# Performance work log

Measured on AMD Instinct MI355X. Metric: run time of the kernel, lower is better.

Reference implementation:

```python
import jax, jax.numpy as jnp
import numpy as np

D = 2048  # input_dim == hidden_dim (mult=1)
B = 16
C = 8.0   # self.c


def setup_inputs() -> dict:
    key = jax.random.key(0)
    k = jax.random.split(key, 5)
    # kaiming_normal fan_in, sigmoid gain = 1 -> std = 1/sqrt(fan_in)
    Wa = jax.random.normal(k[0], (D, D), dtype=jnp.float32) / np.sqrt(D)
    Wx = jax.random.normal(k[1], (D, D), dtype=jnp.float32) / np.sqrt(D)
    ba = jnp.zeros((D,), dtype=jnp.float32)
    bx = jnp.zeros((D,), dtype=jnp.float32)
    lo, hi = float(np.log(0.9 / 0.1)), float(np.log(0.999 / 0.001))  # logit(0.9), logit(0.999)
    Lam = jax.random.uniform(k[2], (D,), dtype=jnp.float32, minval=lo, maxval=hi)
    xt = jax.random.normal(k[3], (B, D), dtype=jnp.float32)
    ht_minus_1 = jax.random.normal(k[4], (B, D), dtype=jnp.float32)
    return {"xt": xt, "ht_minus_1": ht_minus_1, "Wa": Wa, "Wx": Wx,
            "ba": ba, "bx": bx, "Lam": Lam}


def reference(xt, ht_minus_1, Wa, Wx, ba, bx, Lam):
    # gates
    rt = jax.nn.sigmoid(xt @ Wa.T + ba)            # [B, H]
    it = jax.nn.sigmoid(xt @ Wx.T + bx)            # [B, H]
    log_a = -jax.nn.softplus(-Lam)                 # [H]
    a = jnp.exp(log_a * rt / C)                    # [B, H]
    # diag_embed(a): [B, H, H] with a on the diagonal (faithful to torch code)
    at = a[:, :, None] * jnp.eye(D, dtype=a.dtype)
    u = jnp.sqrt(1.0 - a * a) * (it * xt)          # [B, H]
    # torch broadcasting: [B,H,H] * [B,H] -> ht_minus_1/u broadcast over rows
    ht = at * ht_minus_1[:, None, :] + u[:, None, :]  # [B, H, H]
    return ht
```

## Files before the change

### kernel.cpp

```cpp
#include <hip/hip_runtime.h>

#define DD 2048
#define BB 16

typedef float f32x4 __attribute__((ext_vector_type(4)));
typedef short bf16x8 __attribute__((ext_vector_type(8)));

static __device__ inline short bfbits(float f) {
    __bf16 h = (__bf16)f;
    return __builtin_bit_cast(short, h);
}

static __device__ inline bf16x8 cvt8(f32x4 a, f32x4 b) {
    bf16x8 r;
#pragma unroll
    for (int e = 0; e < 4; ++e) {
        r[e]     = bfbits(a[e]);
        r[4 + e] = bfbits(b[e]);
    }
    return r;
}

__global__ __launch_bounds__(512) void gemm_kernel(
    const float* __restrict__ xt,
    const float* __restrict__ Wa, const float* __restrict__ Wx,
    const float* __restrict__ ba, const float* __restrict__ bx,
    float* __restrict__ rawA, float* __restrict__ rawX)
{
    const int gate = blockIdx.x & 1;
    const int jt   = blockIdx.x >> 1;
    const int wv   = threadIdx.x >> 6;
    const int lane = threadIdx.x & 63;
    const int mn   = lane & 15;
    const int kc   = lane >> 4;

    const float* W = gate ? Wx : Wa;
    const float* wrow = W  + (size_t)(jt * 16 + mn) * DD;
    const float* xrow = xt + (size_t)mn * DD;
    const int kbase = wv * 256 + kc * 8;

    f32x4 acc = {0.f, 0.f, 0.f, 0.f};
#pragma unroll
    for (int s = 0; s < 8; ++s) {
        const int k = kbase + s * 32;
        const f32x4 wa0 = *(const f32x4*)(wrow + k);
        const f32x4 wa1 = *(const f32x4*)(wrow + k + 4);
        const f32x4 xb0 = *(const f32x4*)(xrow + k);
        const f32x4 xb1 = *(const f32x4*)(xrow + k + 4);
        const bf16x8 af  = cvt8(wa0, wa1);
        const bf16x8 bf_ = cvt8(xb0, xb1);
        acc = __builtin_amdgcn_mfma_f32_16x16x32_bf16(af, bf_, acc, 0, 0, 0);
    }

    __shared__ float part[8][256];
#pragma unroll
    for (int r = 0; r < 4; ++r) part[wv][lane * 4 + r] = acc[r];
    __syncthreads();

    if (threadIdx.x < 256) {
        const int t = threadIdx.x;
        float s = 0.f;
#pragma unroll
        for (int w = 0; w < 8; ++w) s += part[w][t];
        const int l   = t >> 2;
        const int r   = t & 3;
        const int row = ((l >> 4) << 2) + r;
        const int col = l & 15;
        const int j   = jt * 16 + row;
        s += (gate ? bx : ba)[j];
        (gate ? rawX : rawA)[col * DD + j] = s;
    }
}

__global__ __launch_bounds__(256) void finalize_kernel(
    const float* __restrict__ xt, const float* __restrict__ h,
    const float* __restrict__ Lam,
    float* __restrict__ rawA_u, float* __restrict__ rawX_dv)
{
    const int g = blockIdx.x * 256 + threadIdx.x;
    const int b = g >> 11;
    const int j = g & (DD - 1);

    const float sA = rawA_u[g];
    const float sX = rawX_dv[g];
    const float rt  = 1.f / (1.f + expf(-sA));
    const float itg = 1.f / (1.f + expf(-sX));
    const float log_a = -log1pf(expf(-Lam[j]));
    const float a = expf(log_a * rt * 0.125f);
    const float u = sqrtf(fmaxf(0.f, 1.f - a * a)) * (itg * xt[b * DD + j]);
    const float dv = fmaf(a, h[b * DD + j], u);
    rawA_u[g]  = u;
    rawX_dv[g] = dv;
}

__global__ __launch_bounds__(256) void fill_kernel(
    const float4* __restrict__ u4, const float* __restrict__ dv,
    float4* __restrict__ out)
{
    const int blk = blockIdx.x;
    const int b   = blk >> 8;
    const int ig  = blk & 255;
    const int i0  = ig << 3;
    const int t   = threadIdx.x;

    const float4 v0 = u4[(b << 9) + t];
    const float4 v1 = u4[(b << 9) + 256 + t];

    float4* orow = out + ((size_t)b << 20) + ((size_t)i0 << 9);
#pragma unroll
    for (int r = 0; r < 8; ++r) {
        const int i   = i0 + r;
        const int dj4 = i >> 2;
        float4 w0 = v0, w1 = v1;
        if (dj4 == t) {
            ((float*)&w0)[i & 3] = dv[(b << 11) + i];
        } else if (dj4 == 256 + t) {
            ((float*)&w1)[i & 3] = dv[(b << 11) + i];
        }
        orow[t]       = w0;
        orow[256 + t] = w1;
        orow += DD / 4;
    }
}

extern "C" void kernel_launch(void* const* d_in, const int* in_sizes, int n_in,
                              void* d_out, int out_size, void* d_ws, size_t ws_size,
                              hipStream_t stream) {
    const float* xt  = (const float*)d_in[0];
    const float* h   = (const float*)d_in[1];
    const float* Wa  = (const float*)d_in[2];
    const float* Wx  = (const float*)d_in[3];
    const float* ba  = (const float*)d_in[4];
    const float* bx  = (const float*)d_in[5];
    const float* Lam = (const float*)d_in[6];

    float* rawA = (float*)d_ws;
    float* rawX = rawA + BB * DD;

    gemm_kernel<<<256, 512, 0, stream>>>(xt, Wa, Wx, ba, bx, rawA, rawX);
    finalize_kernel<<<BB * DD / 256, 256, 0, stream>>>(xt, h, Lam, rawA, rawX);
    fill_kernel<<<BB * (DD / 8), 256, 0, stream>>>((const float4*)rawA, rawX, (float4*)d_out);
}
```

Baseline: 61.41 us.

## Fuse gate epilogue into GEMM by pairing Wa and Wx rows per block

Result: no change. 60.24 us (median of 2 runs) (-1.9%).

```diff
diff --git a/kernel.cpp b/kernel.cpp
--- a/kernel.cpp
+++ b/kernel.cpp
@@ -22,20 +22,20 @@
 }
 
 __global__ __launch_bounds__(512) void gemm_kernel(
-    const float* __restrict__ xt,
+    const float* __restrict__ xt, const float* __restrict__ h,
     const float* __restrict__ Wa, const float* __restrict__ Wx,
     const float* __restrict__ ba, const float* __restrict__ bx,
-    float* __restrict__ rawA, float* __restrict__ rawX)
+    const float* __restrict__ Lam,
+    float* __restrict__ u_ws, float* __restrict__ dv_ws)
 {
-    const int gate = blockIdx.x & 1;
-    const int jt   = blockIdx.x >> 1;
+    const int j0   = blockIdx.x * 8;
     const int wv   = threadIdx.x >> 6;
     const int lane = threadIdx.x & 63;
     const int mn   = lane & 15;
     const int kc   = lane >> 4;
 
-    const float* W = gate ? Wx : Wa;
-    const float* wrow = W  + (size_t)(jt * 16 + mn) * DD;
+    const float* wrow = (mn < 8) ? (Wa + (size_t)(j0 + mn) * DD)
+                                 : (Wx + (size_t)(j0 + (mn & 7)) * DD);
     const float* xrow = xt + (size_t)mn * DD;
     const int kbase = wv * 256 + kc * 8;
 
@@ -47,9 +47,7 @@
         const f32x4 wa1 = *(const f32x4*)(wrow + k + 4);
         const f32x4 xb0 = *(const f32x4*)(xrow + k);
         const f32x4 xb1 = *(const f32x4*)(xrow + k + 4);
-        const bf16x8 af  = cvt8(wa0, wa1);
-        const bf16x8 bf_ = cvt8(xb0, xb1);
-        acc = __builtin_amdgcn_mfma_f32_16x16x32_bf16(af, bf_, acc, 0, 0, 0);
+        acc = __builtin_amdgcn_mfma_f32_16x16x32_bf16(cvt8(wa0, wa1), cvt8(xb0, xb1), acc, 0, 0, 0);
     }
 
     __shared__ float part[8][256];
@@ -57,6 +55,7 @@
     for (int r = 0; r < 4; ++r) part[wv][lane * 4 + r] = acc[r];
     __syncthreads();
 
+    __shared__ float comb[16][17];
     if (threadIdx.x < 256) {
         const int t = threadIdx.x;
         float s = 0.f;
@@ -66,31 +65,25 @@
         const int r   = t & 3;
         const int row = ((l >> 4) << 2) + r;
         const int col = l & 15;
-        const int j   = jt * 16 + row;
-        s += (gate ? bx : ba)[j];
-        (gate ? rawX : rawA)[col * DD + j] = s;
+        comb[row][col] = s;
     }
-}
+    __syncthreads();
 
-__global__ __launch_bounds__(256) void finalize_kernel(
-    const float* __restrict__ xt, const float* __restrict__ h,
-    const float* __restrict__ Lam,
-    float* __restrict__ rawA_u, float* __restrict__ rawX_dv)
-{
-    const int g = blockIdx.x * 256 + threadIdx.x;
-    const int b = g >> 11;
-    const int j = g & (DD - 1);
-
-    const float sA = rawA_u[g];
-    const float sX = rawX_dv[g];
-    const float rt  = 1.f / (1.f + expf(-sA));
-    const float itg = 1.f / (1.f + expf(-sX));
-    const float log_a = -log1pf(expf(-Lam[j]));
-    const float a = expf(log_a * rt * 0.125f);
-    const float u = sqrtf(fmaxf(0.f, 1.f - a * a)) * (itg * xt[b * DD + j]);
-    const float dv = fmaf(a, h[b * DD + j], u);
-    rawA_u[g]  = u;
-    rawX_dv[g] = dv;
+    if (threadIdx.x < 128) {
+        const int b  = threadIdx.x >> 3;
+        const int jr = threadIdx.x & 7;
+        const int j  = j0 + jr;
+        const float sA = comb[jr][b]     + ba[j];
+        const float sX = comb[jr + 8][b] + bx[j];
+        const float rt  = 1.f / (1.f + expf(-sA));
+        const float itg = 1.f / (1.f + expf(-sX));
+        const float log_a = -log1pf(expf(-Lam[j]));
+        const float a = expf(log_a * rt * 0.125f);
+        const float u = sqrtf(fmaxf(0.f, 1.f - a * a)) * (itg * xt[b * DD + j]);
+        const float dv = fmaf(a, h[b * DD + j], u);
+        u_ws[b * DD + j]  = u;
+        dv_ws[b * DD + j] = dv;
+    }
 }
 
 __global__ __launch_bounds__(256) void fill_kernel(
@@ -134,10 +127,9 @@
     const float* bx  = (const float*)d_in[5];
     const float* Lam = (const float*)d_in[6];
 
-    float* rawA = (float*)d_ws;
-    float* rawX = rawA + BB * DD;
+    float* u_ws  = (float*)d_ws;
+    float* dv_ws = u_ws + BB * DD;
 
-    gemm_kernel<<<256, 512, 0, stream>>>(xt, Wa, Wx, ba, bx, rawA, rawX);
-    finalize_kernel<<<BB * DD / 256, 256, 0, stream>>>(xt, h, Lam, rawA, rawX);
-    fill_kernel<<<BB * (DD / 8), 256, 0, stream>>>((const float4*)rawA, rawX, (float4*)d_out);
+    gemm_kernel<<<DD / 8, 512, 0, stream>>>(xt, h, Wa, Wx, ba, bx, Lam, u_ws, dv_ws);
+    fill_kernel<<<BB * (DD / 8), 256, 0, stream>>>((const float4*)u_ws, dv_ws, (float4*)d_out);
 }
```
